# Optimization experiments

Hardware: AMD Instinct MI355X
Metric: run time of the kernel (lower is better)

Reference implementation:

```python
import jax, jax.numpy as jnp
import numpy as np

T, B, H, V, D = 128, 16, 8, 25, 64


def setup_inputs() -> dict:
    key = jax.random.key(0)
    k1, k2, k3 = jax.random.split(key, 3)
    q = jax.random.uniform(k1, (T, B, H, V, D), dtype=jnp.float32)
    kv = jax.random.uniform(k2, (T, B, H, V, D), dtype=jnp.float32)
    # decay factor in (0,1), per-head per-channel, as in the torch module
    decay = jax.random.uniform(k3, (1, 1, H, 1, D), dtype=jnp.float32)
    return {"q": q, "kv": kv, "decay": decay}


def reference(q, kv, decay):
    """Decay-based linear recurrent state-space scan (RetNet-style):
        S_t = decay * S_{t-1} + (1 - decay) * kv_t
        out_t = q_t * S_t
    q, kv: (T, B, H, V, D); decay: (1, 1, H, 1, D).
    """
    d = decay[0, 0]          # (H, 1, D), broadcasts against (B, H, V, D)
    one_minus_d = 1.0 - d

    def step(S, qkv_t):
        q_t, kv_t = qkv_t
        S = d * S + one_minus_d * kv_t
        return S, q_t * S

    S0 = jnp.zeros(q.shape[1:], dtype=q.dtype)  # (B, H, V, D)
    _, out = jax.lax.scan(step, S0, (q, kv))
    return out
```

## Files before the change

kernel.cpp:

```cpp
#include <hip/hip_runtime.h>


#define T_DIM 128
#define B_DIM 16
#define H_DIM 8
#define V_DIM 25
#define D_DIM 64
#define CH (B_DIM * H_DIM * V_DIM * D_DIM)

__global__ __launch_bounds__(256) void sss_scan_kernel(
    const float* __restrict__ q,
    const float* __restrict__ kv,
    const float* __restrict__ decay,
    float* __restrict__ out)
{
    const int i = blockIdx.x * blockDim.x + threadIdx.x;
    if (i >= CH) return;

    const int dd = i & (D_DIM - 1);
    const int h  = (i / (V_DIM * D_DIM)) % H_DIM;
    const float d   = decay[h * D_DIM + dd];
    const float omd = 1.0f - d;

    const float* __restrict__ qp = q  + i;
    const float* __restrict__ kp = kv + i;
    float*       __restrict__ op = out + i;

    float S = 0.0f;
    #pragma unroll 4
    for (int t = 0; t < T_DIM; ++t) {
        const size_t off = (size_t)t * CH;
        const float kvt = kp[off];
        const float qt  = qp[off];
        S = fmaf(d, S, omd * kvt);
        op[off] = qt * S;
    }
}

extern "C" void kernel_launch(void* const* d_in, const int* in_sizes, int n_in,
                              void* d_out, int out_size, void* d_ws, size_t ws_size,
                              hipStream_t stream) {
    const float* q     = (const float*)d_in[0];
    const float* kv    = (const float*)d_in[1];
    const float* decay = (const float*)d_in[2];
    float* out = (float*)d_out;

    const int threads = 256;
    const int blocks  = (CH + threads - 1) / threads;
    sss_scan_kernel<<<blocks, threads, 0, stream>>>(q, kv, decay, out);
}
```

Baseline: 257.9 us.

## Vectorize scan to float4 per thread with register double-buffered time prefetch

Each thread now handles four contiguous channels using float4 loads and stores. Inputs for the next four time steps are prefetched into registers while the current four are computed, so more memory requests are in flight per thread. Blocks shrink to 64 threads, and the grid becomes 800 blocks of one wave each. This gives fewer threads in total (51200) and higher register use per thread, which may lower the occupancy available to hide the latency of this bandwidth-bound stream.

```diff
diff --git a/kernel.cpp b/kernel.cpp
--- a/kernel.cpp
+++ b/kernel.cpp
@@ -2,50 +2,74 @@
 
 
 #define T_DIM 128
-#define B_DIM 16
-#define H_DIM 8
-#define V_DIM 25
-#define D_DIM 64
-#define CH (B_DIM * H_DIM * V_DIM * D_DIM)
+#define CH   204800
+#define CH4  (CH / 4)
+#define VD   (25 * 64)
 
-__global__ __launch_bounds__(256) void sss_scan_kernel(
-    const float* __restrict__ q,
-    const float* __restrict__ kv,
-    const float* __restrict__ decay,
-    float* __restrict__ out)
+__global__ __launch_bounds__(64) void sss_scan_v4(
+    const float4* __restrict__ q,
+    const float4* __restrict__ kv,
+    const float*  __restrict__ decay,
+    float4* __restrict__ out)
 {
-    const int i = blockIdx.x * blockDim.x + threadIdx.x;
-    if (i >= CH) return;
+    const int i  = blockIdx.x * 64 + threadIdx.x;
+    const int e0 = i * 4;
+    const int dd = e0 & 63;
+    const int h  = (e0 / VD) & 7;
 
-    const int dd = i & (D_DIM - 1);
-    const int h  = (i / (V_DIM * D_DIM)) % H_DIM;
-    const float d   = decay[h * D_DIM + dd];
-    const float omd = 1.0f - d;
+    const float4 d   = *(const float4*)(decay + h * 64 + dd);
+    const float4 omd = make_float4(1.0f - d.x, 1.0f - d.y, 1.0f - d.z, 1.0f - d.w);
 
-    const float* __restrict__ qp = q  + i;
-    const float* __restrict__ kp = kv + i;
-    float*       __restrict__ op = out + i;
+    const float4* __restrict__ qp = q  + i;
+    const float4* __restrict__ kp = kv + i;
+    float4*       __restrict__ op = out + i;
 
-    float S = 0.0f;
-    #pragma unroll 4
-    for (int t = 0; t < T_DIM; ++t) {
-        const size_t off = (size_t)t * CH;
-        const float kvt = kp[off];
-        const float qt  = qp[off];
-        S = fmaf(d, S, omd * kvt);
-        op[off] = qt * S;
+    float4 S = make_float4(0.f, 0.f, 0.f, 0.f);
+
+    float4 qa[4], ka[4], qb[4], kb[4];
+
+    #pragma unroll
+    for (int j = 0; j < 4; ++j) {
+        ka[j] = kp[(size_t)j * CH4];
+        qa[j] = qp[(size_t)j * CH4];
+    }
+
+    for (int g = 0; g < T_DIM / 4; ++g) {
+        if (g + 1 < T_DIM / 4) {
+            const int tb = (g + 1) * 4;
+            #pragma unroll
+            for (int j = 0; j < 4; ++j) {
+                kb[j] = kp[(size_t)(tb + j) * CH4];
+                qb[j] = qp[(size_t)(tb + j) * CH4];
+            }
+        }
+        #pragma unroll
+        for (int j = 0; j < 4; ++j) {
+            S.x = fmaf(d.x, S.x, omd.x * ka[j].x);
+            S.y = fmaf(d.y, S.y, omd.y * ka[j].y);
+            S.z = fmaf(d.z, S.z, omd.z * ka[j].z);
+            S.w = fmaf(d.w, S.w, omd.w * ka[j].w);
+            float4 o;
+            o.x = qa[j].x * S.x;
+            o.y = qa[j].y * S.y;
+            o.z = qa[j].z * S.z;
+            o.w = qa[j].w * S.w;
+            op[(size_t)(g * 4 + j) * CH4] = o;
+        }
+        #pragma unroll
+        for (int j = 0; j < 4; ++j) { ka[j] = kb[j]; qa[j] = qb[j]; }
     }
 }
 
 extern "C" void kernel_launch(void* const* d_in, const int* in_sizes, int n_in,
                               void* d_out, int out_size, void* d_ws, size_t ws_size,
                               hipStream_t stream) {
-    const float* q     = (const float*)d_in[0];
-    const float* kv    = (const float*)d_in[1];
-    const float* decay = (const float*)d_in[2];
-    float* out = (float*)d_out;
+    const float4* q     = (const float4*)d_in[0];
+    const float4* kv    = (const float4*)d_in[1];
+    const float*  decay = (const float*)d_in[2];
+    float4* out = (float4*)d_out;
 
-    const int threads = 256;
-    const int blocks  = (CH + threads - 1) / threads;
-    sss_scan_kernel<<<blocks, threads, 0, stream>>>(q, kv, decay, out);
+    const int threads = 64;
+    const int blocks  = CH4 / threads;
+    sss_scan_v4<<<blocks, threads, 0, stream>>>(q, kv, decay, out);
 }
```

Result: no change. 256.2 us (-0.7%).

## Split time scan into chunks with cross-chunk parallel prefix in shared memory

Applied to the files above, without the earlier changes.

Each block now handles 64 channels with 8 warps, each warp scanning a 16-step time chunk locally. Chunk carry states are combined with a Hillis-Steele prefix in shared memory using powers of the decay, and a second pass applies the carry-in and writes the output. This exposes 8x more parallelism to hide memory latency on the long sequential scan. In exchange it adds block syncs, shared memory and a register array per thread, and kv and q are each read in a separate pass.

```diff
diff --git a/kernel.cpp b/kernel.cpp
--- a/kernel.cpp
+++ b/kernel.cpp
@@ -1,39 +1,65 @@
 #include <hip/hip_runtime.h>
 
 
-#define T_DIM 128
-#define B_DIM 16
-#define H_DIM 8
-#define V_DIM 25
-#define D_DIM 64
-#define CH (B_DIM * H_DIM * V_DIM * D_DIM)
+#define T_DIM    128
+#define CH       204800
+#define VD       1600
+#define C_CHUNKS 8
+#define L_CHUNK  16
 
-__global__ __launch_bounds__(256) void sss_scan_kernel(
+__global__ __launch_bounds__(512) void sss_scan_chunked(
     const float* __restrict__ q,
     const float* __restrict__ kv,
     const float* __restrict__ decay,
     float* __restrict__ out)
 {
-    const int i = blockIdx.x * blockDim.x + threadIdx.x;
-    if (i >= CH) return;
+    const int lane = threadIdx.x & 63;
+    const int c    = threadIdx.x >> 6;
+    const int ch   = blockIdx.x * 64 + lane;
 
-    const int dd = i & (D_DIM - 1);
-    const int h  = (i / (V_DIM * D_DIM)) % H_DIM;
-    const float d   = decay[h * D_DIM + dd];
+    const int h = (ch / VD) & 7;
+    const float d   = decay[h * 64 + lane];
     const float omd = 1.0f - d;
 
-    const float* __restrict__ qp = q  + i;
-    const float* __restrict__ kp = kv + i;
-    float*       __restrict__ op = out + i;
+    const size_t base = (size_t)(c * L_CHUNK) * CH + ch;
+    const float* __restrict__ kp = kv  + base;
+    const float* __restrict__ qp = q   + base;
+    float*       __restrict__ op = out + base;
 
+    float Sloc[L_CHUNK];
     float S = 0.0f;
-    #pragma unroll 4
-    for (int t = 0; t < T_DIM; ++t) {
-        const size_t off = (size_t)t * CH;
-        const float kvt = kp[off];
-        const float qt  = qp[off];
-        S = fmaf(d, S, omd * kvt);
-        op[off] = qt * S;
+    #pragma unroll
+    for (int j = 0; j < L_CHUNK; ++j) {
+        const float k = kp[j * CH];
+        S = fmaf(d, S, omd * k);
+        Sloc[j] = S;
+    }
+
+    float Q = d * d;  Q *= Q;  Q *= Q;  Q *= Q;
+
+    __shared__ float A[C_CHUNKS][64];
+    A[c][lane] = S;
+    float y  = S;
+    float Qs = Q;
+    #pragma unroll
+    for (int s = 1; s < C_CHUNKS; s <<= 1) {
+        __syncthreads();
+        const float prev = (c >= s) ? A[c - s][lane] : 0.0f;
+        __syncthreads();
+        y = fmaf(Qs, prev, y);
+        A[c][lane] = y;
+        Qs *= Qs;
+    }
+    __syncthreads();
+    const float Sin = (c > 0) ? A[c - 1][lane] : 0.0f;
+
+    float r = Sin;
+    #pragma unroll
+    for (int j = 0; j < L_CHUNK; ++j) {
+        const float qv = qp[j * CH];
+        r *= d;
+        const float Strue = Sloc[j] + r;
+        op[j * CH] = qv * Strue;
     }
 }
 
@@ -45,7 +71,7 @@
     const float* decay = (const float*)d_in[2];
     float* out = (float*)d_out;
 
-    const int threads = 256;
-    const int blocks  = (CH + threads - 1) / threads;
-    sss_scan_kernel<<<blocks, threads, 0, stream>>>(q, kv, decay, out);
+    const int threads = 512;
+    const int blocks  = CH / 64;
+    sss_scan_chunked<<<blocks, threads, 0, stream>>>(q, kv, decay, out);
 }
```

New measurement: 262.5 us. No clear change (+1.8%).
